# Kernel tuning notes

Hardware: AMD Instinct MI355X
Metric: run time of the kernel (lower is better)

## Reference

```python
import jax, jax.numpy as jnp
import numpy as np

B, N, C = 8, 1024, 256
H = 8
D = C // H
PARAM_DIM = 16
EPS = 1e-5


def layernorm(x, g, b):
    m = jnp.mean(x, axis=-1, keepdims=True)
    v = jnp.mean((x - m) ** 2, axis=-1, keepdims=True)
    return (x - m) * jax.lax.rsqrt(v + EPS) * g + b


def setup_inputs() -> dict:
    key = jax.random.key(0)
    ks = jax.random.split(key, 12)
    s = 0.02
    return {
        "img_tokens": jax.random.normal(ks[0], (B, N, C), jnp.float32),
        "param_tokens": jax.random.normal(ks[1], (B, PARAM_DIM), jnp.float32),
        "img_norm_g": jnp.ones((C,), jnp.float32),
        "img_norm_b": jnp.zeros((C,), jnp.float32),
        "Wq": jax.random.normal(ks[2], (C, C), jnp.float32) * s,
        "Wparam": jax.random.normal(ks[3], (PARAM_DIM, C), jnp.float32) * s,
        "bparam": jnp.zeros((C,), jnp.float32),
        "ctx_norm_g": jnp.ones((C,), jnp.float32),
        "ctx_norm_b": jnp.zeros((C,), jnp.float32),
        "Wkv": jax.random.normal(ks[4], (C, 2 * C), jnp.float32) * s,
        "Wout": jax.random.normal(ks[5], (C, C), jnp.float32) * s,
        "bout": jnp.zeros((C,), jnp.float32),
    }


def reference(img_tokens, param_tokens, img_norm_g, img_norm_b, Wq, Wparam,
              bparam, ctx_norm_g, ctx_norm_b, Wkv, Wout, bout):
    # queries from normalized image tokens: [B, N, C]
    q = layernorm(img_tokens, img_norm_g, img_norm_b) @ Wq
    # single context token per sample: [B, C]
    ctx = param_tokens @ Wparam + bparam
    kv = layernorm(ctx, ctx_norm_g, ctx_norm_b) @ Wkv  # [B, 2C]
    k, v = kv[:, :C], kv[:, C:]

    qh = q.reshape(B, N, H, D).transpose(0, 2, 1, 3)  # [B, H, N, D]
    kh = k.reshape(B, H, D)                           # one key token per head
    vh = v.reshape(B, H, D)

    scale = 1.0 / jnp.sqrt(jnp.asarray(D, jnp.float32))
    # each query scores the same key; original expands it N times -> rows constant
    scores = jnp.einsum('bhnd,bhd->bhn', qh, kh) * scale        # [B, H, N]
    scores_full = jnp.broadcast_to(scores[:, :, :, None], (B, H, N, N))
    attn = jax.nn.softmax(scores_full, axis=-1)                  # uniform rows
    v_full = jnp.broadcast_to(vh[:, :, None, :], (B, H, N, D))   # identical values
    out = jnp.einsum('bhnm,bhmd->bhnd', attn, v_full)            # [B, H, N, D]

    out = out.transpose(0, 2, 1, 3).reshape(B, N, C)
    out = out @ Wout + bout
    return out + img_tokens
```

## Files before the change

### kernel.cpp

```cpp
#include <hip/hip_runtime.h>
#include <math.h>

#define BB 8
#define NN 1024
#define CC 256
#define PARAM_DIM 16
#define EPS 1e-5f

__device__ __forceinline__ float block_sum(float x, float* red) {
    #pragma unroll
    for (int o = 32; o > 0; o >>= 1) x += __shfl_down(x, o, 64);
    __syncthreads();
    if ((threadIdx.x & 63) == 0) red[threadIdx.x >> 6] = x;
    __syncthreads();
    return red[0] + red[1] + red[2] + red[3];
}

__global__ __launch_bounds__(CC) void compute_y_kernel(
    const float* __restrict__ param,
    const float* __restrict__ Wparam,
    const float* __restrict__ bparam,
    const float* __restrict__ ctx_g,
    const float* __restrict__ ctx_b,
    const float* __restrict__ Wkv,
    const float* __restrict__ Wout,
    const float* __restrict__ bout,
    float* __restrict__ y)
{
    const int b = blockIdx.x;
    const int c = threadIdx.x;

    __shared__ float sm[CC];
    __shared__ float red[4];
    __shared__ float p[PARAM_DIM];

    if (c < PARAM_DIM) p[c] = param[b * PARAM_DIM + c];
    __syncthreads();

    float ctx = bparam[c];
    #pragma unroll
    for (int j = 0; j < PARAM_DIM; ++j)
        ctx = fmaf(p[j], Wparam[j * CC + c], ctx);

    float mean = block_sum(ctx, red) * (1.0f / CC);
    float d = ctx - mean;
    float var = block_sum(d * d, red) * (1.0f / CC);
    float ln = d * rsqrtf(var + EPS) * ctx_g[c] + ctx_b[c];

    __syncthreads();
    sm[c] = ln;
    __syncthreads();

    float v = 0.0f;
    #pragma unroll 8
    for (int j = 0; j < CC; ++j)
        v = fmaf(sm[j], Wkv[j * (2 * CC) + CC + c], v);

    __syncthreads();
    sm[c] = v;
    __syncthreads();

    float o = bout[c];
    #pragma unroll 8
    for (int j = 0; j < CC; ++j)
        o = fmaf(sm[j], Wout[j * CC + c], o);

    y[b * CC + c] = o;
}

__global__ __launch_bounds__(256) void bcast_add_kernel(
    const float4* __restrict__ img4,
    const float4* __restrict__ y4,
    float4* __restrict__ out4)
{
    const int i4 = blockIdx.x * blockDim.x + threadIdx.x;
    const int b  = i4 >> 16;
    const int c4 = i4 & 63;
    float4 a = img4[i4];
    float4 yy = y4[b * 64 + c4];
    a.x += yy.x; a.y += yy.y; a.z += yy.z; a.w += yy.w;
    out4[i4] = a;
}

extern "C" void kernel_launch(void* const* d_in, const int* in_sizes, int n_in,
                              void* d_out, int out_size, void* d_ws, size_t ws_size,
                              hipStream_t stream) {
    const float* img     = (const float*)d_in[0];
    const float* param   = (const float*)d_in[1];
    const float* Wparam  = (const float*)d_in[5];
    const float* bparam  = (const float*)d_in[6];
    const float* ctx_g   = (const float*)d_in[7];
    const float* ctx_b   = (const float*)d_in[8];
    const float* Wkv     = (const float*)d_in[9];
    const float* Wout    = (const float*)d_in[10];
    const float* bout    = (const float*)d_in[11];
    float* out = (float*)d_out;
    float* y   = (float*)d_ws;

    compute_y_kernel<<<BB, CC, 0, stream>>>(param, Wparam, bparam, ctx_g, ctx_b,
                                            Wkv, Wout, bout, y);

    const int total4 = BB * NN * CC / 4;
    bcast_add_kernel<<<total4 / 256, 256, 0, stream>>>(
        (const float4*)img, (const float4*)y, (float4*)out);
}
```

Before: 105.3 us.

## Split-K the tiny GEMVs across 1024 threads with float4 weight loads

The per-sample kernel that computes the constant output vector now launches 1024 threads per block instead of 256. The two 256x256 matrix-vector products are split into 16 K-slices, each thread handles four output columns with float4 loads, and the partials are reduced through shared memory. The point is to shorten the long serial dependent FMA chain in a kernel that runs only 8 blocks and sits on the critical path before the broadcast add. The layernorm statistics are computed over 4 replicated copies and divided by 1024, which gives the same mean. The cost is more shared memory and extra barriers.

```diff
diff --git a/kernel.cpp b/kernel.cpp
--- a/kernel.cpp
+++ b/kernel.cpp
@@ -7,16 +7,8 @@
 #define PARAM_DIM 16
 #define EPS 1e-5f
 
-__device__ __forceinline__ float block_sum(float x, float* red) {
-    #pragma unroll
-    for (int o = 32; o > 0; o >>= 1) x += __shfl_down(x, o, 64);
-    __syncthreads();
-    if ((threadIdx.x & 63) == 0) red[threadIdx.x >> 6] = x;
-    __syncthreads();
-    return red[0] + red[1] + red[2] + red[3];
-}
 
-__global__ __launch_bounds__(CC) void compute_y_kernel(
+__global__ __launch_bounds__(1024) void compute_y_kernel(
     const float* __restrict__ param,
     const float* __restrict__ Wparam,
     const float* __restrict__ bparam,
@@ -27,14 +19,19 @@
     const float* __restrict__ bout,
     float* __restrict__ y)
 {
-    const int b = blockIdx.x;
-    const int c = threadIdx.x;
+    const int b  = blockIdx.x;
+    const int t  = threadIdx.x;
+    const int c  = t & 255;
+    const int c4 = t & 63;
+    const int k  = t >> 6;
 
-    __shared__ float sm[CC];
-    __shared__ float red[4];
-    __shared__ float p[PARAM_DIM];
+    __shared__ float  sln[CC];
+    __shared__ float  sv[CC];
+    __shared__ float4 smp[1024];
+    __shared__ float  red[16];
+    __shared__ float  p[PARAM_DIM];
 
-    if (c < PARAM_DIM) p[c] = param[b * PARAM_DIM + c];
+    if (t < PARAM_DIM) p[t] = param[b * PARAM_DIM + t];
     __syncthreads();
 
     float ctx = bparam[c];
@@ -42,30 +39,83 @@
     for (int j = 0; j < PARAM_DIM; ++j)
         ctx = fmaf(p[j], Wparam[j * CC + c], ctx);
 
-    float mean = block_sum(ctx, red) * (1.0f / CC);
-    float d = ctx - mean;
-    float var = block_sum(d * d, red) * (1.0f / CC);
-    float ln = d * rsqrtf(var + EPS) * ctx_g[c] + ctx_b[c];
+    float s = ctx;
+    #pragma unroll
+    for (int o = 32; o > 0; o >>= 1) s += __shfl_down(s, o, 64);
+    if ((t & 63) == 0) red[t >> 6] = s;
+    __syncthreads();
+    float tot = 0.0f;
+    #pragma unroll
+    for (int i = 0; i < 16; ++i) tot += red[i];
+    const float mean = tot * (1.0f / 1024.0f);
 
+    const float d = ctx - mean;
+    float s2 = d * d;
     __syncthreads();
-    sm[c] = ln;
+    #pragma unroll
+    for (int o = 32; o > 0; o >>= 1) s2 += __shfl_down(s2, o, 64);
+    if ((t & 63) == 0) red[t >> 6] = s2;
+    __syncthreads();
+    tot = 0.0f;
+    #pragma unroll
+    for (int i = 0; i < 16; ++i) tot += red[i];
+    const float var = tot * (1.0f / 1024.0f);
+
+    const float ln = d * rsqrtf(var + EPS) * ctx_g[c] + ctx_b[c];
+    if (t < CC) sln[c] = ln;
     __syncthreads();
 
-    float v = 0.0f;
-    #pragma unroll 8
-    for (int j = 0; j < CC; ++j)
-        v = fmaf(sm[j], Wkv[j * (2 * CC) + CC + c], v);
-
+    const float4* __restrict__ Wkv4 = (const float4*)Wkv;
+    float4 acc = make_float4(0.f, 0.f, 0.f, 0.f);
+    #pragma unroll
+    for (int jj = 0; jj < 16; ++jj) {
+        const int j = k * 16 + jj;
+        const float a = sln[j];
+        const float4 w = Wkv4[j * 128 + 64 + c4];
+        acc.x = fmaf(a, w.x, acc.x);
+        acc.y = fmaf(a, w.y, acc.y);
+        acc.z = fmaf(a, w.z, acc.z);
+        acc.w = fmaf(a, w.w, acc.w);
+    }
+    smp[t] = acc;
     __syncthreads();
-    sm[c] = v;
+    if (t < 64) {
+        float4 r = smp[c4];
+        #pragma unroll
+        for (int kk = 1; kk < 16; ++kk) {
+            const float4 q = smp[kk * 64 + c4];
+            r.x += q.x; r.y += q.y; r.z += q.z; r.w += q.w;
+        }
+        sv[c4 * 4 + 0] = r.x; sv[c4 * 4 + 1] = r.y;
+        sv[c4 * 4 + 2] = r.z; sv[c4 * 4 + 3] = r.w;
+    }
     __syncthreads();
 
-    float o = bout[c];
-    #pragma unroll 8
-    for (int j = 0; j < CC; ++j)
-        o = fmaf(sm[j], Wout[j * CC + c], o);
-
-    y[b * CC + c] = o;
+    const float4* __restrict__ Wout4 = (const float4*)Wout;
+    acc = make_float4(0.f, 0.f, 0.f, 0.f);
+    #pragma unroll
+    for (int jj = 0; jj < 16; ++jj) {
+        const int j = k * 16 + jj;
+        const float a = sv[j];
+        const float4 w = Wout4[j * 64 + c4];
+        acc.x = fmaf(a, w.x, acc.x);
+        acc.y = fmaf(a, w.y, acc.y);
+        acc.z = fmaf(a, w.z, acc.z);
+        acc.w = fmaf(a, w.w, acc.w);
+    }
+    smp[t] = acc;
+    __syncthreads();
+    if (t < 64) {
+        float4 r = smp[c4];
+        #pragma unroll
+        for (int kk = 1; kk < 16; ++kk) {
+            const float4 q = smp[kk * 64 + c4];
+            r.x += q.x; r.y += q.y; r.z += q.z; r.w += q.w;
+        }
+        const float4 bo = ((const float4*)bout)[c4];
+        r.x += bo.x; r.y += bo.y; r.z += bo.z; r.w += bo.w;
+        ((float4*)y)[b * 64 + c4] = r;
+    }
 }
 
 __global__ __launch_bounds__(256) void bcast_add_kernel(
@@ -77,7 +127,7 @@
     const int b  = i4 >> 16;
     const int c4 = i4 & 63;
     float4 a = img4[i4];
-    float4 yy = y4[b * 64 + c4];
+    const float4 yy = y4[b * 64 + c4];
     a.x += yy.x; a.y += yy.y; a.z += yy.z; a.w += yy.w;
     out4[i4] = a;
 }
@@ -97,8 +147,8 @@
     float* out = (float*)d_out;
     float* y   = (float*)d_ws;
 
-    compute_y_kernel<<<BB, CC, 0, stream>>>(param, Wparam, bparam, ctx_g, ctx_b,
-                                            Wkv, Wout, bout, y);
+    compute_y_kernel<<<BB, 1024, 0, stream>>>(param, Wparam, bparam, ctx_g, ctx_b,
+                                              Wkv, Wout, bout, y);
 
     const int total4 = BB * NN * CC / 4;
     bcast_add_kernel<<<total4 / 256, 256, 0, stream>>>(
```

Result: faster. 91.19 us (-13.4%).
